# Optimization experiments

Hardware: AMD Instinct MI355X
Metric: run time of the kernel (lower is better)

## Reference

```python
import jax, jax.numpy as jnp
import numpy as np

GAMMA = 0.9865


def setup_inputs() -> dict:
    key = jax.random.key(0)
    ks = jax.random.split(key, 6)
    B, T, DIN, D = 8, 2048, 1024, 1024
    return {
        "xq": jax.random.normal(ks[0], (B, T, DIN), dtype=jnp.float32),
        "xk": jax.random.normal(ks[1], (B, T, DIN), dtype=jnp.float32),
        "xv": jax.random.normal(ks[2], (B, T, DIN), dtype=jnp.float32),
        "Wq": jax.random.normal(ks[3], (DIN, D), dtype=jnp.float32) * (DIN ** -0.5),
        "Wk": jax.random.normal(ks[4], (DIN, D), dtype=jnp.float32) * (DIN ** -0.5),
        "Wv": jax.random.normal(ks[5], (DIN, D), dtype=jnp.float32) * (DIN ** -0.5),
    }


def reference(xq, xk, xv, Wq, Wk, Wv):
    # Dense projections (no bias)
    Q = jnp.einsum("btd,de->bte", xq, Wq)  # [B,T,D]
    K = jnp.einsum("btd,de->bte", xk, Wk)
    V = jnp.einsum("btd,de->bte", xv, Wv)

    # einsum('ib,bj->bj', K_t^T, V_t) == (sum_i K[b,t,i]) * V[b,t,:]
    ksum = jnp.sum(K, axis=-1)            # [B,T]
    u = ksum[..., None] * V               # [B,T,D]
    # recurrence starts at t=1 with s[0]=0, so u[0] never contributes
    u = u * (jnp.arange(u.shape[1]) > 0)[None, :, None]

    def step(s, u_t):
        s = s * jnp.float32(GAMMA) + u_t
        return s, s

    s0 = jnp.zeros(u.shape[::2], dtype=u.dtype)          # [B,D]
    _, S = jax.lax.scan(step, s0, jnp.swapaxes(u, 0, 1))  # S: [T,B,D]
    return Q * jnp.swapaxes(S, 0, 1)                      # [B,T,D]
```

## Files before the change

### kernel.cpp

```cpp
#include <hip/hip_runtime.h>
#include <hip/hip_bf16.h>

#define GAMMA 0.9865f

typedef __attribute__((ext_vector_type(8))) short bf16x8;
typedef __attribute__((ext_vector_type(4))) float f32x4;

static constexpr int Bb  = 8;
static constexpr int Tt  = 2048;
static constexpr int DIN = 1024;
static constexpr int Dd  = 1024;
static constexpr int Mm  = Bb * Tt;
static constexpr int CL  = 64;
static constexpr int NC  = Tt / CL;
static constexpr int NT  = DIN / 64;

__device__ __forceinline__ void gload16(const void* g, void* l) {
  __builtin_amdgcn_global_load_lds(
      (const __attribute__((address_space(1))) void*)g,
      (__attribute__((address_space(3))) void*)l, 16, 0, 0);
}

__device__ __forceinline__ void bar() {
  asm volatile("" ::: "memory");
  __builtin_amdgcn_s_barrier();
  asm volatile("" ::: "memory");
}

__device__ __forceinline__ float bf16_to_f32(unsigned short u) {
  return __uint_as_float(((unsigned int)u) << 16);
}

__global__ __launch_bounds__(256) void prep_kernel(
    const float* __restrict__ Wq, const float* __restrict__ Wk,
    const float* __restrict__ Wv, float* __restrict__ wsum,
    __hip_bfloat16* __restrict__ Wt) {
  int bid = blockIdx.x;
  if (bid < 256) {
    int row  = bid * 4 + (threadIdx.x >> 6);
    int lane = threadIdx.x & 63;
    const float4* rp = (const float4*)(Wk + (size_t)row * DIN);
    float s = 0.f;
#pragma unroll
    for (int i = 0; i < 4; ++i) {
      float4 v = rp[lane + i * 64];
      s += v.x + v.y + v.z + v.w;
    }
    for (int off = 32; off; off >>= 1) s += __shfl_down(s, off);
    if (lane == 0) wsum[row] = s;
    return;
  }
  int wid = bid - 256;
  int z = wid >> 10, rem = wid & 1023;
  int kb = rem & 31, nb = rem >> 5;
  const float* W = z ? Wv : Wq;
  __hip_bfloat16* outp = Wt + (size_t)z * DIN * Dd;
  __shared__ float tile[32][33];
  int k0 = kb * 32, n0 = nb * 32;
  int tx = threadIdx.x & 31, ty = threadIdx.x >> 5;
#pragma unroll
  for (int i = 0; i < 4; ++i)
    tile[ty + i * 8][tx] = W[(size_t)(k0 + ty + i * 8) * Dd + n0 + tx];
  __syncthreads();
#pragma unroll
  for (int i = 0; i < 4; ++i)
    outp[(size_t)(n0 + ty + i * 8) * DIN + k0 + tx] =
        __float2bfloat16(tile[tx][ty + i * 8]);
}

__global__ __launch_bounds__(256) void castksum_kernel(
    const float* __restrict__ xq, const float* __restrict__ xk,
    const float* __restrict__ xv, const float* __restrict__ wsum,
    __hip_bfloat16* __restrict__ oq, __hip_bfloat16* __restrict__ ov,
    float* __restrict__ ksum) {
  int y = blockIdx.y;
  if (y < 2) {
    const float* src = y ? xv : xq;
    __hip_bfloat16* dst = y ? ov : oq;
    size_t i = (size_t)blockIdx.x * 256 + threadIdx.x;
    const float4* p = (const float4*)src;
    float4 a = p[i * 2], b = p[i * 2 + 1];
    union { __hip_bfloat16 h[8]; bf16x8 v; } u;
    u.h[0] = __float2bfloat16(a.x); u.h[1] = __float2bfloat16(a.y);
    u.h[2] = __float2bfloat16(a.z); u.h[3] = __float2bfloat16(a.w);
    u.h[4] = __float2bfloat16(b.x); u.h[5] = __float2bfloat16(b.y);
    u.h[6] = __float2bfloat16(b.z); u.h[7] = __float2bfloat16(b.w);
    ((bf16x8*)dst)[i] = u.v;
    return;
  }
  if (blockIdx.x >= Mm / 4) return;
  int row  = blockIdx.x * 4 + (threadIdx.x >> 6);
  int lane = threadIdx.x & 63;
  const float4* rp = (const float4*)(xk + (size_t)row * DIN);
  const float4* wp = (const float4*)wsum;
  float s = 0.f;
#pragma unroll
  for (int i = 0; i < 4; ++i) {
    float4 a = rp[lane + i * 64];
    float4 w = wp[lane + i * 64];
    s += a.x * w.x + a.y * w.y + a.z * w.z + a.w * w.w;
  }
  for (int off = 32; off; off >>= 1) s += __shfl_down(s, off);
  if (lane == 0) ksum[row] = s;
}

__device__ __forceinline__ void stage_half(const __hip_bfloat16* g, char* l, int tid) {
#pragma unroll
  for (int j = 0; j < 2; ++j) {
    int c = tid + j * 512;
    int row = c >> 3, ch = c & 7;
    gload16(g + (size_t)row * DIN + ((ch ^ (row & 7)) << 3), l + c * 16);
  }
}

__device__ __forceinline__ bf16x8 lds_frag(const char* base, int row, int kc) {
  return *(const bf16x8*)(base + (((row << 3) + (kc ^ (row & 7))) << 4));
}

#define MFMA_QUAD(MLO, NLO)                                                  \
  _Pragma("unroll") for (int mi = 0; mi < 4; ++mi)                           \
  _Pragma("unroll") for (int ni = 0; ni < 2; ++ni)                           \
  _Pragma("unroll") for (int ks = 0; ks < 2; ++ks)                           \
      acc[(MLO) + mi][(NLO) + ni] = __builtin_amdgcn_mfma_f32_16x16x32_bf16( \
          a[(MLO) + mi][ks], b[(NLO) + ni][ks], acc[(MLO) + mi][(NLO) + ni], 0, 0, 0);

__device__ __forceinline__ void gemm_core(const __hip_bfloat16* Ag,
                                          const __hip_bfloat16* Bg, char* lds,
                                          int tid, int wm, int wn, int fq, int fr,
                                          f32x4 (&acc)[8][4]) {
  stage_half(Ag,                  lds,                 tid);
  stage_half(Ag + 128 * DIN,      lds + 16384,         tid);
  stage_half(Bg,                  lds + 32768,         tid);
  stage_half(Bg + 128 * DIN,      lds + 49152,         tid);
  stage_half(Ag + 64,             lds + 65536,         tid);
  stage_half(Ag + 128 * DIN + 64, lds + 65536 + 16384, tid);
  asm volatile("s_waitcnt vmcnt(4)" ::: "memory");
  bar();

  for (int t = 0; t < NT; ++t) {
    char* buf  = lds + (t & 1) * 65536;
    char* bufN = lds + ((t + 1) & 1) * 65536;
    const char* At = buf;
    const char* Bt = buf + 32768;
    bf16x8 a[8][2], b[4][2];

#pragma unroll
    for (int mi = 0; mi < 4; ++mi)
#pragma unroll
      for (int ks = 0; ks < 2; ++ks)
        a[mi][ks] = lds_frag(At, wm + mi * 16 + fr, ks * 4 + fq);
#pragma unroll
    for (int ni = 0; ni < 2; ++ni)
#pragma unroll
      for (int ks = 0; ks < 2; ++ks)
        b[ni][ks] = lds_frag(Bt, wn + ni * 16 + fr, ks * 4 + fq);
    if (t + 1 < NT) stage_half(Bg + (size_t)(t + 1) * 64, bufN + 32768, tid);
    bar();
    __builtin_amdgcn_s_setprio(1);
    MFMA_QUAD(0, 0);
    __builtin_amdgcn_s_setprio(0);
    bar();

#pragma unroll
    for (int mi = 4; mi < 8; ++mi)
#pragma unroll
      for (int ks = 0; ks < 2; ++ks)
        a[mi][ks] = lds_frag(At, wm + mi * 16 + fr, ks * 4 + fq);
    if (t + 1 < NT)
      stage_half(Bg + 128 * DIN + (size_t)(t + 1) * 64, bufN + 49152, tid);
    bar();
    __builtin_amdgcn_s_setprio(1);
    MFMA_QUAD(4, 0);
    __builtin_amdgcn_s_setprio(0);
    bar();

#pragma unroll
    for (int ni = 2; ni < 4; ++ni)
#pragma unroll
      for (int ks = 0; ks < 2; ++ks)
        b[ni][ks] = lds_frag(Bt, wn + ni * 16 + fr, ks * 4 + fq);
    if (t + 2 < NT) stage_half(Ag + (size_t)(t + 2) * 64, buf, tid);
    bar();
    __builtin_amdgcn_s_setprio(1);
    MFMA_QUAD(0, 2);
    __builtin_amdgcn_s_setprio(0);
    bar();

    if (t + 2 < NT)
      stage_half(Ag + 128 * DIN + (size_t)(t + 2) * 64, buf + 16384, tid);
    if (t + 1 < NT) {
      if (t + 2 < NT) asm volatile("s_waitcnt vmcnt(4)" ::: "memory");
      else            asm volatile("s_waitcnt vmcnt(0)" ::: "memory");
    }
    bar();
    __builtin_amdgcn_s_setprio(1);
    MFMA_QUAD(4, 2);
    __builtin_amdgcn_s_setprio(0);
    bar();
  }
}

__global__ __launch_bounds__(512, 2) void gemmV_kernel(
    const __hip_bfloat16* __restrict__ Av, const __hip_bfloat16* __restrict__ Wt,
    const float* __restrict__ ksum, __hip_bfloat16* __restrict__ Vbf,
    float* __restrict__ E) {
  extern __shared__ char lds[];
  int lin = blockIdx.x;
  int wg  = (lin & 7) * 32 + (lin >> 3);
  int by  = wg & 3, bx = wg >> 2;
  const int m0 = bx * 256, n0 = by * 256;
  const __hip_bfloat16* Ag = Av + (size_t)m0 * DIN;
  const __hip_bfloat16* Bg = Wt + ((size_t)Dd + n0) * DIN;

  const int tid = threadIdx.x;
  const int wv = tid >> 6, lane = tid & 63;
  const int wm = (wv >> 2) * 128, wn = (wv & 3) * 64;
  const int fq = lane >> 4, fr = lane & 15;

  f32x4 acc[8][4] = {};
  gemm_core(Ag, Bg, lds, tid, wm, wn, fq, fr, acc);

#pragma unroll
  for (int mi = 0; mi < 8; ++mi) {
#pragma unroll
    for (int ni = 0; ni < 4; ++ni) {
      f32x4 v = acc[mi][ni];
      int row = wm + mi * 16 + fq * 4;
      int col = wn + ni * 16 + fr;
#pragma unroll
      for (int j = 0; j < 4; ++j) {
        int r = row + j;
        unsigned short h = __bfloat16_as_ushort(__float2bfloat16(v[j]));
        Vbf[(size_t)(m0 + r) * Dd + n0 + col] = __ushort_as_bfloat16(h);
        *(unsigned short*)(lds + r * 512 + ((col * 2) ^ ((r & 7) << 4))) = h;
      }
    }
  }
  bar();

  const int b = m0 >> 11, t0 = m0 & 2047;
#pragma unroll
  for (int p = 0; p < 2; ++p) {
    int task = tid + p * 512;
    int col = task & 255, cc = task >> 8;
    const float* kp = ksum + (size_t)b * Tt + t0 + cc * 64;
    float s = 0.f;
    for (int i = 0; i < CL; ++i) {
      int t = cc * 64 + i;
      float v = bf16_to_f32(
          *(const unsigned short*)(lds + t * 512 + ((col * 2) ^ ((t & 7) << 4))));
      float kv = kp[i];
      if (t0 == 0 && cc == 0 && i == 0) kv = 0.f;
      s = s * GAMMA + kv * v;
    }
    E[((size_t)b * NC + (t0 >> 6) + cc) * Dd + n0 + col] = s;
  }
}

__global__ __launch_bounds__(512, 2) void gemmQ_kernel(
    const __hip_bfloat16* __restrict__ Aq, const __hip_bfloat16* __restrict__ Wt,
    const __hip_bfloat16* __restrict__ Vbf, const float* __restrict__ ksum,
    const float* __restrict__ carry, float* __restrict__ outp) {
  extern __shared__ char lds[];
  int lin = blockIdx.x;
  int wg  = (lin & 7) * 32 + (lin >> 3);
  int by  = wg & 3, bx = wg >> 2;
  const int m0 = bx * 256, n0 = by * 256;
  const __hip_bfloat16* Ag = Aq + (size_t)m0 * DIN;
  const __hip_bfloat16* Bg = Wt + (size_t)n0 * DIN;

  const int tid = threadIdx.x;
  const int wv = tid >> 6, lane = tid & 63;
  const int wm = (wv >> 2) * 128, wn = (wv & 3) * 64;
  const int fq = lane >> 4, fr = lane & 15;

  f32x4 acc[8][4] = {};
  gemm_core(Ag, Bg, lds, tid, wm, wn, fq, fr, acc);

  const int b = m0 >> 11, t0 = m0 & 2047;
#pragma unroll
  for (int j = 0; j < 16; ++j) {
    int c = tid + j * 512;
    int row = c >> 5, s = c & 31;
    int chn = s ^ (row & 7);
    gload16(Vbf + (size_t)(m0 + row) * Dd + n0 + chn * 8, lds + c * 16);
  }
  asm volatile("s_waitcnt vmcnt(0)" ::: "memory");
  bar();

#pragma unroll
  for (int p = 0; p < 2; ++p) {
    int task = tid + p * 512;
    int col = task & 255, cc = task >> 8;
    float s = carry[((size_t)b * NC + (t0 >> 6) + cc) * Dd + n0 + col];
    const float* kp = ksum + (size_t)b * Tt + t0 + cc * 64;
    for (int i = 0; i < CL; ++i) {
      int t = cc * 64 + i;
      int addr = t * 512 + ((col * 2) ^ ((t & 7) << 4));
      unsigned short* sp = (unsigned short*)(lds + addr);
      float v = bf16_to_f32(*sp);
      float kv = kp[i];
      if (t0 == 0 && cc == 0 && i == 0) kv = 0.f;
      s = s * GAMMA + kv * v;
      *sp = __bfloat16_as_ushort(__float2bfloat16(s));
    }
  }
  bar();

#pragma unroll
  for (int mi = 0; mi < 8; ++mi) {
#pragma unroll
    for (int ni = 0; ni < 4; ++ni) {
      f32x4 v = acc[mi][ni];
      int row = wm + mi * 16 + fq * 4;
      int col = wn + ni * 16 + fr;
#pragma unroll
      for (int j = 0; j < 4; ++j) {
        int r = row + j;
        float S = bf16_to_f32(
            *(const unsigned short*)(lds + r * 512 + ((col * 2) ^ ((r & 7) << 4))));
        outp[(size_t)(m0 + r) * Dd + n0 + col] = v[j] * S;
      }
    }
  }
}

__global__ void scanB_kernel(const float* __restrict__ E, float* __restrict__ carry,
                             float gCL) {
  int b = blockIdx.x;
  int d = blockIdx.y * 256 + threadIdx.x;
  float send = 0.f;
  for (int c = 0; c < NC; ++c) {
    size_t idx = ((size_t)b * NC + c) * Dd + d;
    float e = E[idx];
    carry[idx] = send;
    send = e + gCL * send;
  }
}

extern "C" void kernel_launch(void* const* d_in, const int* in_sizes, int n_in,
                              void* d_out, int out_size, void* d_ws, size_t ws_size,
                              hipStream_t stream) {
  (void)in_sizes; (void)n_in; (void)out_size; (void)ws_size;
  const float* xq = (const float*)d_in[0];
  const float* xk = (const float*)d_in[1];
  const float* xv = (const float*)d_in[2];
  const float* Wq = (const float*)d_in[3];
  const float* Wk = (const float*)d_in[4];
  const float* Wv = (const float*)d_in[5];
  float* outp = (float*)d_out;

  char* ws = (char*)d_ws;
  size_t off = 0;
  auto alloc = [&](size_t bytes) {
    char* p = ws + off;
    off += (bytes + 255) & ~(size_t)255;
    return p;
  };
  __hip_bfloat16* xq_bf = (__hip_bfloat16*)alloc((size_t)Mm * DIN * 2);
  __hip_bfloat16* xv_bf = (__hip_bfloat16*)alloc((size_t)Mm * DIN * 2);
  __hip_bfloat16* Wt    = (__hip_bfloat16*)alloc((size_t)2 * DIN * Dd * 2);
  __hip_bfloat16* Vbf   = (__hip_bfloat16*)alloc((size_t)Mm * Dd * 2);
  float* wsum  = (float*)alloc((size_t)DIN * 4);
  float* ksum  = (float*)alloc((size_t)Mm * 4);
  float* E     = (float*)alloc((size_t)Bb * NC * Dd * 4);
  float* carry = (float*)alloc((size_t)Bb * NC * Dd * 4);

  double g = 1.0;
  for (int i = 0; i < CL; ++i) g *= (double)GAMMA;
  float gCL = (float)g;

  (void)hipFuncSetAttribute((const void*)gemmV_kernel,
                            hipFuncAttributeMaxDynamicSharedMemorySize, 131072);
  (void)hipFuncSetAttribute((const void*)gemmQ_kernel,
                            hipFuncAttributeMaxDynamicSharedMemorySize, 131072);

  prep_kernel<<<256 + 2048, 256, 0, stream>>>(Wq, Wk, Wv, wsum, Wt);
  castksum_kernel<<<dim3(Mm * DIN / 8 / 256, 3), 256, 0, stream>>>(
      xq, xk, xv, wsum, xq_bf, xv_bf, ksum);
  gemmV_kernel<<<256, 512, 131072, stream>>>(xv_bf, Wt, ksum, Vbf, E);
  scanB_kernel<<<dim3(Bb, Dd / 256), 256, 0, stream>>>(E, carry, gCL);
  gemmQ_kernel<<<256, 512, 131072, stream>>>(xq_bf, Wt, Vbf, ksum, carry, outp);
}
```

Before: 143.6 us.

## Fuse chunk-carry scan into gemmQ and prefetch V tile during GEMM tail

Removes the separate scan kernel and its carry buffer; each gemmQ block now recomputes its chunk carry by serially scanning the E chunk totals in its prologue. The V tile load into LDS is issued during the final GEMM iteration instead of after it, overlapping that load with the last MFMAs. This saves one launch and a global round trip. In exchange, every block does redundant serial work of up to 31 dependent loads per thread before its GEMM starts.

```diff
diff --git a/kernel.cpp b/kernel.cpp
--- a/kernel.cpp
+++ b/kernel.cpp
@@ -113,6 +113,17 @@
   }
 }
 
+__device__ __forceinline__ void stageV_half(const __hip_bfloat16* Vt, char* lds,
+                                            int tid, int h) {
+#pragma unroll
+  for (int j = 0; j < 8; ++j) {
+    int c = tid + (h * 8 + j) * 512;
+    int row = c >> 5, sl = c & 31;
+    int chn = sl ^ (row & 7);
+    gload16(Vt + (size_t)row * Dd + chn * 8, lds + c * 16);
+  }
+}
+
 __device__ __forceinline__ bf16x8 lds_frag(const char* base, int row, int kc) {
   return *(const bf16x8*)(base + (((row << 3) + (kc ^ (row & 7))) << 4));
 }
@@ -124,8 +135,10 @@
       acc[(MLO) + mi][(NLO) + ni] = __builtin_amdgcn_mfma_f32_16x16x32_bf16( \
           a[(MLO) + mi][ks], b[(NLO) + ni][ks], acc[(MLO) + mi][(NLO) + ni], 0, 0, 0);
 
+template <bool STAGEV>
 __device__ __forceinline__ void gemm_core(const __hip_bfloat16* Ag,
-                                          const __hip_bfloat16* Bg, char* lds,
+                                          const __hip_bfloat16* Bg,
+                                          const __hip_bfloat16* Vt, char* lds,
                                           int tid, int wm, int wn, int fq, int fr,
                                           f32x4 (&acc)[8][4]) {
   stage_half(Ag,                  lds,                 tid);
@@ -155,6 +168,7 @@
       for (int ks = 0; ks < 2; ++ks)
         b[ni][ks] = lds_frag(Bt, wn + ni * 16 + fr, ks * 4 + fq);
     if (t + 1 < NT) stage_half(Bg + (size_t)(t + 1) * 64, bufN + 32768, tid);
+    else if (STAGEV) stageV_half(Vt, lds, tid, 0);
     bar();
     __builtin_amdgcn_s_setprio(1);
     MFMA_QUAD(0, 0);
@@ -188,6 +202,8 @@
 
     if (t + 2 < NT)
       stage_half(Ag + 128 * DIN + (size_t)(t + 2) * 64, buf + 16384, tid);
+    else if (STAGEV && t + 1 >= NT)
+      stageV_half(Vt, lds, tid, 1);
     if (t + 1 < NT) {
       if (t + 2 < NT) asm volatile("s_waitcnt vmcnt(4)" ::: "memory");
       else            asm volatile("s_waitcnt vmcnt(0)" ::: "memory");
@@ -218,7 +234,7 @@
   const int fq = lane >> 4, fr = lane & 15;
 
   f32x4 acc[8][4] = {};
-  gemm_core(Ag, Bg, lds, tid, wm, wn, fq, fr, acc);
+  gemm_core<false>(Ag, Bg, nullptr, lds, tid, wm, wn, fq, fr, acc);
 
 #pragma unroll
   for (int mi = 0; mi < 8; ++mi) {
@@ -260,7 +276,7 @@
 __global__ __launch_bounds__(512, 2) void gemmQ_kernel(
     const __hip_bfloat16* __restrict__ Aq, const __hip_bfloat16* __restrict__ Wt,
     const __hip_bfloat16* __restrict__ Vbf, const float* __restrict__ ksum,
-    const float* __restrict__ carry, float* __restrict__ outp) {
+    const float* __restrict__ E, float gCL, float* __restrict__ outp) {
   extern __shared__ char lds[];
   int lin = blockIdx.x;
   int wg  = (lin & 7) * 32 + (lin >> 3);
@@ -268,23 +284,32 @@
   const int m0 = bx * 256, n0 = by * 256;
   const __hip_bfloat16* Ag = Aq + (size_t)m0 * DIN;
   const __hip_bfloat16* Bg = Wt + (size_t)n0 * DIN;
+  const int b = m0 >> 11, t0 = m0 & 2047;
 
   const int tid = threadIdx.x;
   const int wv = tid >> 6, lane = tid & 63;
   const int wm = (wv >> 2) * 128, wn = (wv & 3) * 64;
   const int fq = lane >> 4, fr = lane & 15;
 
+  float carryR[2];
+  {
+    const int cbase = t0 >> 6;
+#pragma unroll
+    for (int p = 0; p < 2; ++p) {
+      int task = tid + p * 512;
+      int col = task & 255, cc = task >> 8;
+      int C = cbase + cc;
+      float s = 0.f;
+      for (int j = 0; j < C; ++j)
+        s = E[((size_t)b * NC + j) * Dd + n0 + col] + gCL * s;
+      carryR[p] = s;
+    }
+  }
+
   f32x4 acc[8][4] = {};
-  gemm_core(Ag, Bg, lds, tid, wm, wn, fq, fr, acc);
-
-  const int b = m0 >> 11, t0 = m0 & 2047;
-#pragma unroll
-  for (int j = 0; j < 16; ++j) {
-    int c = tid + j * 512;
-    int row = c >> 5, s = c & 31;
-    int chn = s ^ (row & 7);
-    gload16(Vbf + (size_t)(m0 + row) * Dd + n0 + chn * 8, lds + c * 16);
-  }
+  gemm_core<true>(Ag, Bg, Vbf + (size_t)m0 * Dd + n0, lds,
+                  tid, wm, wn, fq, fr, acc);
+
   asm volatile("s_waitcnt vmcnt(0)" ::: "memory");
   bar();
 
@@ -292,7 +317,7 @@
   for (int p = 0; p < 2; ++p) {
     int task = tid + p * 512;
     int col = task & 255, cc = task >> 8;
-    float s = carry[((size_t)b * NC + (t0 >> 6) + cc) * Dd + n0 + col];
+    float s = carryR[p];
     const float* kp = ksum + (size_t)b * Tt + t0 + cc * 64;
     for (int i = 0; i < CL; ++i) {
       int t = cc * 64 + i;
@@ -322,19 +347,6 @@
         outp[(size_t)(m0 + r) * Dd + n0 + col] = v[j] * S;
       }
     }
-  }
-}
-
-__global__ void scanB_kernel(const float* __restrict__ E, float* __restrict__ carry,
-                             float gCL) {
-  int b = blockIdx.x;
-  int d = blockIdx.y * 256 + threadIdx.x;
-  float send = 0.f;
-  for (int c = 0; c < NC; ++c) {
-    size_t idx = ((size_t)b * NC + c) * Dd + d;
-    float e = E[idx];
-    carry[idx] = send;
-    send = e + gCL * send;
   }
 }
 
@@ -364,7 +376,6 @@
   float* wsum  = (float*)alloc((size_t)DIN * 4);
   float* ksum  = (float*)alloc((size_t)Mm * 4);
   float* E     = (float*)alloc((size_t)Bb * NC * Dd * 4);
-  float* carry = (float*)alloc((size_t)Bb * NC * Dd * 4);
 
   double g = 1.0;
   for (int i = 0; i < CL; ++i) g *= (double)GAMMA;
@@ -379,6 +390,5 @@
   castksum_kernel<<<dim3(Mm * DIN / 8 / 256, 3), 256, 0, stream>>>(
       xq, xk, xv, wsum, xq_bf, xv_bf, ksum);
   gemmV_kernel<<<256, 512, 131072, stream>>>(xv_bf, Wt, ksum, Vbf, E);
-  scanB_kernel<<<dim3(Bb, Dd / 256), 256, 0, stream>>>(E, carry, gCL);
-  gemmQ_kernel<<<256, 512, 131072, stream>>>(xq_bf, Wt, Vbf, ksum, carry, outp);
-}
+  gemmQ_kernel<<<256, 512, 131072, stream>>>(xq_bf, Wt, Vbf, ksum, E, gCL, outp);
+}
```

New measurement: 143.9 us. About the same (+0.2%).
